# Kernel optimization log

Measured on AMD Instinct MI355X. Metric: run time of the kernel, lower is better.

## Reference

```python
import jax, jax.numpy as jnp
import numpy as np

S, H, HEADS = 2048, 1024, 16   # seq_len, hidden_size, num attention heads
E, NM, P = 256, 1024, 2048     # num entities, total mentions, num candidate pairs
PH = 1024                      # pair_hidden_size


def setup_inputs() -> dict:
    key = jax.random.key(0)
    ks = jax.random.split(key, 13)
    s = 1.0 / np.sqrt(H)
    return {
        "sequence_output": jax.random.normal(ks[0], (S, H), jnp.float32),
        "attention": jax.random.uniform(ks[1], (HEADS, S, S), jnp.float32),
        "mention_idx": jax.random.randint(ks[2], (NM,), 0, S, jnp.int32),
        "entity_ids": jnp.sort(jax.random.randint(ks[3], (NM,), 0, E, jnp.int32)),
        "pair_h": jax.random.randint(ks[4], (P,), 0, E, jnp.int32),
        "pair_t": jax.random.randint(ks[5], (P,), 0, E, jnp.int32),
        "W_head": jax.random.normal(ks[6], (H, PH), jnp.float32) * s,
        "b_head": jnp.zeros((PH,), jnp.float32),
        "W_tail": jax.random.normal(ks[7], (H, PH), jnp.float32) * s,
        "b_tail": jnp.zeros((PH,), jnp.float32),
        "W_ctx": jax.random.normal(ks[8], (H, PH), jnp.float32) * s,
        "W_bil": jax.random.normal(ks[9], (PH, PH), jnp.float32) * s,
        "b_bil": jnp.zeros((), jnp.float32),
    }


def reference(sequence_output, attention, mention_idx, entity_ids, pair_h, pair_t,
              W_head, b_head, W_tail, b_tail, W_ctx, W_bil, b_bil):
    # ---- entity aggregation: ragged segment logsumexp (embs) + segment mean (atts) ----
    vals = sequence_output[mention_idx]                               # [NM, H]
    counts = jax.ops.segment_sum(jnp.ones((NM,), vals.dtype), entity_ids, num_segments=E)
    has = counts > 0                                                  # [E]
    seg_max = jax.ops.segment_max(vals, entity_ids, num_segments=E)   # [E, H]
    seg_max = jnp.where(has[:, None], seg_max, 0.0)
    sums = jax.ops.segment_sum(jnp.exp(vals - seg_max[entity_ids]), entity_ids, num_segments=E)
    ent_emb = jnp.where(has[:, None],
                        seg_max + jnp.log(jnp.where(has[:, None], sums, 1.0)),
                        0.0)                                          # [E, H]
    m_att = jnp.transpose(attention[:, mention_idx, :], (1, 0, 2))    # [NM, HEADS, S]
    ent_att = jax.ops.segment_sum(m_att, entity_ids, num_segments=E)
    ent_att = ent_att / jnp.maximum(counts, 1.0)[:, None, None]       # [E, HEADS, S]

    # ---- pair scoring ----
    hs, ts = ent_emb[pair_h], ent_emb[pair_t]                         # [P, H]
    pair_att = (ent_att[pair_h] * ent_att[pair_t]).sum(axis=1)        # [P, S]
    pair_att = pair_att / (pair_att.sum(axis=-1, keepdims=True) + 1e-6)
    contexts = pair_att @ sequence_output                             # [P, H]
    ctx_p = contexts @ W_ctx                                          # [P, PH]
    z_s = jnp.tanh(hs @ W_head + b_head + ctx_p)
    z_o = jnp.tanh(ts @ W_tail + b_tail + ctx_p)
    logits = jnp.einsum('pi,ij,pj->p', z_s, W_bil, z_o) + b_bil       # [P]
    return logits
```

## Files before the change

kernel.cpp:

```cpp
#include <hip/hip_runtime.h>
#include <hip/hip_bf16.h>
#include <math.h>
#include <stdint.h>

#define S_LEN  2048
#define HID    1024
#define NHEADS 16
#define NE     256
#define NMEN   1024
#define NP     2048
#define PHID   1024

typedef __attribute__((ext_vector_type(8))) short bf16x8;
typedef __attribute__((ext_vector_type(4))) float f32x4;
typedef unsigned int uint;

__device__ inline void seg_bounds(const int* __restrict__ entity_ids, int e,
                                  int& start, int& end) {
    int lo = 0, hi = NMEN;
    while (lo < hi) { int mid = (lo + hi) >> 1; if (entity_ids[mid] < e) lo = mid + 1; else hi = mid; }
    start = lo;
    hi = NMEN;
    while (lo < hi) { int mid = (lo + hi) >> 1; if (entity_ids[mid] <= e) lo = mid + 1; else hi = mid; }
    end = lo;
}

__device__ __forceinline__ void load_lds16(const void* g, void* l) {
    __builtin_amdgcn_global_load_lds(
        (const __attribute__((address_space(1))) uint32_t*)g,
        (__attribute__((address_space(3))) uint32_t*)l,
        16, 0, 0);
}

__device__ __forceinline__ float bflo(uint u) { return __uint_as_float(u << 16); }
__device__ __forceinline__ float bfhi(uint u) { return __uint_as_float(u & 0xffff0000u); }
__device__ __forceinline__ uint pk2(float a, float b) {
    __hip_bfloat16 ha = __float2bfloat16(a), hb = __float2bfloat16(b);
    unsigned short ua = *(unsigned short*)&ha, ub = *(unsigned short*)&hb;
    return (uint)ua | ((uint)ub << 16);
}

__global__ void prep_ent_kernel(const float* __restrict__ seq,
                                const float* __restrict__ attention,
                                const float* __restrict__ w0, const float* __restrict__ w1,
                                const float* __restrict__ w2, const float* __restrict__ w3,
                                const int* __restrict__ mention_idx,
                                const int* __restrict__ entity_ids,
                                __hip_bfloat16* __restrict__ seqB,
                                __hip_bfloat16* __restrict__ o0, __hip_bfloat16* __restrict__ o1,
                                __hip_bfloat16* __restrict__ o2, __hip_bfloat16* __restrict__ o3,
                                uint2* __restrict__ eaB,
                                __hip_bfloat16* __restrict__ ent_emb)
{
    __shared__ float tbuf[32][33];
    __shared__ int sb[2];
    int id = blockIdx.x;
    if (id < 1024) {
        long i = (long)id * 256 + threadIdx.x;
        const float4* in4 = (const float4*)seq;
        float4 a = in4[2 * i], b = in4[2 * i + 1];
        uint4 o;
        o.x = pk2(a.x, a.y); o.y = pk2(a.z, a.w);
        o.z = pk2(b.x, b.y); o.w = pk2(b.z, b.w);
        ((uint4*)seqB)[i] = o;
        return;
    }
    if (id < 5120) {
        int t = id - 1024;
        int z = t >> 10;
        const float* in = (z == 0) ? w0 : (z == 1) ? w1 : (z == 2) ? w2 : w3;
        __hip_bfloat16* out = (z == 0) ? o0 : (z == 1) ? o1 : (z == 2) ? o2 : o3;
        int r0 = ((t >> 5) & 31) * 32, c0 = (t & 31) * 32;
        int j = threadIdx.x & 31, i0 = threadIdx.x >> 5;
        for (int i = i0; i < 32; i += 8)
            tbuf[i][j] = in[(long)(r0 + i) * 1024 + c0 + j];
        __syncthreads();
        for (int i = i0; i < 32; i += 8)
            out[(long)(c0 + i) * 1024 + r0 + j] = __float2bfloat16(tbuf[j][i]);
        return;
    }
    int t = id - 5120;
    int e = t & 255, role = t >> 8;
    if (threadIdx.x == 0) { int s, tt; seg_bounds(entity_ids, e, s, tt); sb[0] = s; sb[1] = tt; }
    __syncthreads();
    int start = sb[0], end = sb[1];

    if (role < 16) {
        const float4* att4 = (const float4*)attention;
        int h = role;
        float inv = 1.f / fmaxf((float)(end - start), 1.f);
        for (int s4 = threadIdx.x; s4 < S_LEN / 4; s4 += 256) {
            float ax = 0.f, ay = 0.f, az = 0.f, aw = 0.f;
            for (int i = start; i < end; ++i) {
                float4 v = att4[((long)h * S_LEN + mention_idx[i]) * (S_LEN / 4) + s4];
                ax += v.x; ay += v.y; az += v.z; aw += v.w;
            }
            uint2 o; o.x = pk2(ax * inv, ay * inv); o.y = pk2(az * inv, aw * inv);
            eaB[((long)e * NHEADS + h) * (S_LEN / 4) + s4] = o;
        }
    } else {
        const float4* seq4 = (const float4*)seq;
        int col4 = threadIdx.x;
        uint2 o;
        if (end <= start) {
            o.x = 0; o.y = 0;
            ((uint2*)ent_emb)[(long)e * 256 + col4] = o;
            return;
        }
        float mx = -INFINITY, my = -INFINITY, mz = -INFINITY, mw = -INFINITY;
        for (int i = start; i < end; ++i) {
            float4 v = seq4[(long)mention_idx[i] * 256 + col4];
            mx = fmaxf(mx, v.x); my = fmaxf(my, v.y); mz = fmaxf(mz, v.z); mw = fmaxf(mw, v.w);
        }
        float sx = 0.f, sy = 0.f, sz = 0.f, sw = 0.f;
        for (int i = start; i < end; ++i) {
            float4 v = seq4[(long)mention_idx[i] * 256 + col4];
            sx += expf(v.x - mx); sy += expf(v.y - my); sz += expf(v.z - mz); sw += expf(v.w - mw);
        }
        o.x = pk2(mx + logf(sx), my + logf(sy));
        o.y = pk2(mz + logf(sz), mw + logf(sw));
        ((uint2*)ent_emb)[(long)e * 256 + col4] = o;
    }
}

template <int MODE>
__device__ __forceinline__ void gemm_core(
    const __hip_bfloat16* __restrict__ A,
    const __hip_bfloat16* __restrict__ Bt,
    void* __restrict__ Cout, const float* __restrict__ zo, float* __restrict__ out,
    int M, int N, int Kstride, int kLen,
    int bx, int by, int bz,
    short (*As)[128][8], short (*Bs)[128][8])
{
    int tid = threadIdx.x;
    int lane = tid & 63, wid = tid >> 6;
    int wr = wid >> 1, wc = wid & 1;
    int bm = by * 128, bn = bx * 128;
    int kBeg = bz * kLen;

    const __hip_bfloat16* gsrc[8];
    void* ldst[8];
#pragma unroll
    for (int i = 0; i < 8; ++i) {
        int c = wid * 8 + i;
        int isA = (c < 16) ? 1 : 0;
        int cc = isA ? c : c - 16;
        int kg2 = cc >> 1, rh = cc & 1;
        gsrc[i] = (isA ? A + (long)(bm + rh * 64 + lane) * Kstride
                       : Bt + (long)(bn + rh * 64 + lane) * Kstride) + kBeg + kg2 * 8;
        ldst[i] = isA ? (void*)&As[kg2][rh * 64][0] : (void*)&Bs[kg2][rh * 64][0];
    }

    f32x4 acc[4][4] = {};
    int kg = lane >> 4, lr = lane & 15;

    for (int k0 = 0; k0 < kLen; k0 += 64) {
#pragma unroll
        for (int i = 0; i < 8; ++i)
            load_lds16(gsrc[i] + k0, ldst[i]);
        __syncthreads();
#pragma unroll
        for (int sub = 0; sub < 2; ++sub) {
            bf16x8 af[4], bfr[4];
#pragma unroll
            for (int f = 0; f < 4; ++f) {
                af[f]  = *(const bf16x8*)&As[sub * 4 + kg][wr * 64 + f * 16 + lr][0];
                bfr[f] = *(const bf16x8*)&Bs[sub * 4 + kg][wc * 64 + f * 16 + lr][0];
            }
#pragma unroll
            for (int fm = 0; fm < 4; ++fm)
#pragma unroll
                for (int fn = 0; fn < 4; ++fn)
                    acc[fm][fn] = __builtin_amdgcn_mfma_f32_16x16x32_bf16(af[fm], bfr[fn], acc[fm][fn], 0, 0, 0);
        }
        __syncthreads();
    }

    int q4 = (lane >> 4) * 4;
    if (MODE == 0) {
#pragma unroll
        for (int fm = 0; fm < 4; ++fm)
#pragma unroll
            for (int fn = 0; fn < 4; ++fn) {
                int row = bm + wr * 64 + fm * 16 + q4;
                int col = bn + wc * 64 + fn * 16 + lr;
#pragma unroll
                for (int r = 0; r < 4; ++r)
                    ((float*)Cout)[((long)bz * M + row + r) * N + col] = acc[fm][fn][r];
            }
    } else if (MODE == 1) {
#pragma unroll
        for (int fm = 0; fm < 4; ++fm)
#pragma unroll
            for (int fn = 0; fn < 4; ++fn) {
                int row = bm + wr * 64 + fm * 16 + q4;
                int col = bn + wc * 64 + fn * 16 + lr;
#pragma unroll
                for (int r = 0; r < 4; ++r)
                    ((__hip_bfloat16*)Cout)[(long)(row + r) * N + col] = __float2bfloat16(acc[fm][fn][r]);
            }
    } else {
#pragma unroll
        for (int fm = 0; fm < 4; ++fm) {
#pragma unroll
            for (int r = 0; r < 4; ++r) {
                int row = bm + wr * 64 + fm * 16 + q4 + r;
                float v = 0.f;
#pragma unroll
                for (int fn = 0; fn < 4; ++fn) {
                    int col = bn + wc * 64 + fn * 16 + lr;
                    v += acc[fm][fn][r] * zo[(long)row * N + col];
                }
                v += __shfl_xor(v, 1, 64);
                v += __shfl_xor(v, 2, 64);
                v += __shfl_xor(v, 4, 64);
                v += __shfl_xor(v, 8, 64);
                if (lr == 0) atomicAdd(out + row, v);
            }
        }
    }
}

__launch_bounds__(256)
__global__ void pair_seqw_ehet(const __hip_bfloat16* __restrict__ WctxT,
                               const __hip_bfloat16* __restrict__ seqB,
                               __hip_bfloat16* __restrict__ seqWT,
                               const __hip_bfloat16* __restrict__ embB,
                               const __hip_bfloat16* __restrict__ WhtT,
                               float* __restrict__ ehetP,
                               const uint4* __restrict__ ea,
                               const int* __restrict__ pair_h,
                               const int* __restrict__ pair_t,
                               uint4* __restrict__ patt)
{
    __shared__ short As[8][128][8];
    __shared__ short Bs[8][128][8];
    int id = blockIdx.x;
    if (id < 128) {
        gemm_core<1>(WctxT, seqB, seqWT, nullptr, nullptr,
                     PHID, S_LEN, HID, HID, id & 15, id >> 4, 0, As, Bs);
        return;
    }
    if (id < 256) {
        int u = id - 128;
        gemm_core<0>(embB, WhtT, ehetP, nullptr, nullptr,
                     NE, 2 * PHID, HID, HID / 4, u & 15, (u >> 4) & 1, u >> 5, As, Bs);
        return;
    }
    __shared__ float wsum[4];
    int p = id - 256;
    long bh = (long)pair_h[p] * NHEADS * (S_LEN / 8);
    long bt = (long)pair_t[p] * NHEADS * (S_LEN / 8);
    int s8 = threadIdx.x;
    float a0 = 0, a1 = 0, a2 = 0, a3 = 0, a4 = 0, a5 = 0, a6 = 0, a7 = 0;
#pragma unroll
    for (int h = 0; h < NHEADS; ++h) {
        uint4 xa = ea[bh + h * (S_LEN / 8) + s8];
        uint4 xb = ea[bt + h * (S_LEN / 8) + s8];
        a0 += bflo(xa.x) * bflo(xb.x); a1 += bfhi(xa.x) * bfhi(xb.x);
        a2 += bflo(xa.y) * bflo(xb.y); a3 += bfhi(xa.y) * bfhi(xb.y);
        a4 += bflo(xa.z) * bflo(xb.z); a5 += bfhi(xa.z) * bfhi(xb.z);
        a6 += bflo(xa.w) * bflo(xb.w); a7 += bfhi(xa.w) * bfhi(xb.w);
    }
    float psum = a0 + a1 + a2 + a3 + a4 + a5 + a6 + a7;
#pragma unroll
    for (int off = 32; off > 0; off >>= 1)
        psum += __shfl_down(psum, off, 64);
    int lane = threadIdx.x & 63, wid = threadIdx.x >> 6;
    if (lane == 0) wsum[wid] = psum;
    __syncthreads();
    float inv = 1.f / (wsum[0] + wsum[1] + wsum[2] + wsum[3] + 1e-6f);
    uint4 o;
    o.x = pk2(a0 * inv, a1 * inv); o.y = pk2(a2 * inv, a3 * inv);
    o.z = pk2(a4 * inv, a5 * inv); o.w = pk2(a6 * inv, a7 * inv);
    patt[(long)p * (S_LEN / 8) + s8] = o;
}

template <int MODE>
__launch_bounds__(256)
__global__ void gemm_single(const __hip_bfloat16* __restrict__ A,
                            const __hip_bfloat16* __restrict__ Bt,
                            void* __restrict__ Cout,
                            const float* __restrict__ zo,
                            float* __restrict__ out,
                            int M, int N, int Kstride, int kLen)
{
    __shared__ short As[8][128][8];
    __shared__ short Bs[8][128][8];
    gemm_core<MODE>(A, Bt, Cout, zo, out, M, N, Kstride, kLen,
                    blockIdx.x, blockIdx.y, blockIdx.z, As, Bs);
}

__global__ void zs_zo_kernel(const float* __restrict__ ctxpP,
                             const float* __restrict__ ehetP,
                             const float* __restrict__ b_head,
                             const float* __restrict__ b_tail,
                             const int* __restrict__ pair_h,
                             const int* __restrict__ pair_t,
                             __hip_bfloat16* __restrict__ zs, float* __restrict__ zo,
                             const float* __restrict__ b_bil, float* __restrict__ out)
{
    long idx = (long)blockIdx.x * 256 + threadIdx.x;
    if (idx < NP) out[idx] = b_bil[0];
    int p = (int)(idx >> 10);
    int j = (int)(idx & (PHID - 1));
    const long n = (long)NP * PHID;
    float c = ctxpP[idx] + ctxpP[n + idx] + ctxpP[2 * n + idx] + ctxpP[3 * n + idx];
    const long m = (long)NE * 2 * PHID;
    long hb = (long)pair_h[p] * 2048 + j;
    long tb = (long)pair_t[p] * 2048 + 1024 + j;
    float hs = b_head[j] + c, ts = b_tail[j] + c;
#pragma unroll
    for (int s = 0; s < 4; ++s) {
        hs += ehetP[s * m + hb];
        ts += ehetP[s * m + tb];
    }
    zs[idx] = __float2bfloat16(tanhf(hs));
    zo[idx] = tanhf(ts);
}

extern "C" void kernel_launch(void* const* d_in, const int* in_sizes, int n_in,
                              void* d_out, int out_size, void* d_ws, size_t ws_size,
                              hipStream_t stream)
{
    const float* seq        = (const float*)d_in[0];
    const float* attention  = (const float*)d_in[1];
    const int*   mention_idx= (const int*)  d_in[2];
    const int*   entity_ids = (const int*)  d_in[3];
    const int*   pair_h     = (const int*)  d_in[4];
    const int*   pair_t     = (const int*)  d_in[5];
    const float* W_head     = (const float*)d_in[6];
    const float* b_head     = (const float*)d_in[7];
    const float* W_tail     = (const float*)d_in[8];
    const float* b_tail     = (const float*)d_in[9];
    const float* W_ctx      = (const float*)d_in[10];
    const float* W_bil      = (const float*)d_in[11];
    const float* b_bil      = (const float*)d_in[12];
    float* out = (float*)d_out;

    char* w = (char*)d_ws;
    __hip_bfloat16* seqB  = (__hip_bfloat16*)(w + 0);
    __hip_bfloat16* WctxT = (__hip_bfloat16*)(w + (4l << 20));
    __hip_bfloat16* WhtT  = (__hip_bfloat16*)(w + (6l << 20));
    __hip_bfloat16* WbilT = (__hip_bfloat16*)(w + (10l << 20));
    __hip_bfloat16* embB  = (__hip_bfloat16*)(w + (12l << 20));
    __hip_bfloat16* eaB   = (__hip_bfloat16*)(w + (13l << 20));
    __hip_bfloat16* pattB = (__hip_bfloat16*)(w + (29l << 20));
    __hip_bfloat16* seqWT = (__hip_bfloat16*)(w + (37l << 20));
    __hip_bfloat16* zsB   = (__hip_bfloat16*)(w + (41l << 20));
    float* zo    = (float*)(w + (45l << 20));
    float* ctxpP = (float*)(w + (53l << 20));
    float* ehetP = (float*)(w + (85l << 20));

    prep_ent_kernel<<<9472, 256, 0, stream>>>(seq, attention, W_ctx, W_head, W_tail, W_bil,
                                              mention_idx, entity_ids,
                                              seqB, WctxT, WhtT, WhtT + (long)PHID * HID, WbilT,
                                              (uint2*)eaB, embB);

    pair_seqw_ehet<<<2304, 256, 0, stream>>>(WctxT, seqB, seqWT, embB, WhtT, ehetP,
                                             (const uint4*)eaB, pair_h, pair_t, (uint4*)pattB);

    gemm_single<0><<<dim3(8, 16, 4), 256, 0, stream>>>(pattB, seqWT, ctxpP, nullptr, nullptr,
                                                       NP, PHID, S_LEN, S_LEN / 4);

    zs_zo_kernel<<<8192, 256, 0, stream>>>(ctxpP, ehetP, b_head, b_tail, pair_h, pair_t,
                                           zsB, zo, b_bil, out);

    gemm_single<2><<<dim3(8, 16, 2), 256, 0, stream>>>(zsB, WbilT, nullptr, zo, out,
                                                       NP, PHID, HID, HID / 2);
}
```

Measured before the change: 145.8 us.

## Shrink intermediates to bf16, fold ehet split-K reduce into ctxp GEMM launch

The split-K partial outputs of the context GEMM are now stored as bf16 instead of fp32. The four ehet partials are pre-reduced by extra blocks in the same launch as that GEMM, and the blocks are remapped in a swizzled order. zs_zo is vectorised to four elements per thread and writes zo in bf16. W_bil is no longer transposed; the bilinear GEMM instead uses zo as the A operand and untransposed W_bil, with zs as the epilogue vector. The aim is to cut HBM traffic and the transpose work, at the cost of extra bf16 rounding on the partial sums and on zo.

```diff
diff --git a/kernel.cpp b/kernel.cpp
--- a/kernel.cpp
+++ b/kernel.cpp
@@ -43,12 +43,12 @@
 __global__ void prep_ent_kernel(const float* __restrict__ seq,
                                 const float* __restrict__ attention,
                                 const float* __restrict__ w0, const float* __restrict__ w1,
-                                const float* __restrict__ w2, const float* __restrict__ w3,
+                                const float* __restrict__ w2, const float* __restrict__ wbil,
                                 const int* __restrict__ mention_idx,
                                 const int* __restrict__ entity_ids,
                                 __hip_bfloat16* __restrict__ seqB,
                                 __hip_bfloat16* __restrict__ o0, __hip_bfloat16* __restrict__ o1,
-                                __hip_bfloat16* __restrict__ o2, __hip_bfloat16* __restrict__ o3,
+                                __hip_bfloat16* __restrict__ o2, __hip_bfloat16* __restrict__ obil,
                                 uint2* __restrict__ eaB,
                                 __hip_bfloat16* __restrict__ ent_emb)
 {
@@ -65,11 +65,11 @@
         ((uint4*)seqB)[i] = o;
         return;
     }
-    if (id < 5120) {
+    if (id < 4096) {
         int t = id - 1024;
         int z = t >> 10;
-        const float* in = (z == 0) ? w0 : (z == 1) ? w1 : (z == 2) ? w2 : w3;
-        __hip_bfloat16* out = (z == 0) ? o0 : (z == 1) ? o1 : (z == 2) ? o2 : o3;
+        const float* in = (z == 0) ? w0 : (z == 1) ? w1 : w2;
+        __hip_bfloat16* out = (z == 0) ? o0 : (z == 1) ? o1 : o2;
         int r0 = ((t >> 5) & 31) * 32, c0 = (t & 31) * 32;
         int j = threadIdx.x & 31, i0 = threadIdx.x >> 5;
         for (int i = i0; i < 32; i += 8)
@@ -79,7 +79,17 @@
             out[(long)(c0 + i) * 1024 + r0 + j] = __float2bfloat16(tbuf[j][i]);
         return;
     }
-    int t = id - 5120;
+    if (id < 4608) {
+        long i = (long)(id - 4096) * 256 + threadIdx.x;
+        const float4* in4 = (const float4*)wbil;
+        float4 a = in4[2 * i], b = in4[2 * i + 1];
+        uint4 o;
+        o.x = pk2(a.x, a.y); o.y = pk2(a.z, a.w);
+        o.z = pk2(b.x, b.y); o.w = pk2(b.z, b.w);
+        ((uint4*)obil)[i] = o;
+        return;
+    }
+    int t = id - 4608;
     int e = t & 255, role = t >> 8;
     if (threadIdx.x == 0) { int s, tt; seg_bounds(entity_ids, e, s, tt); sb[0] = s; sb[1] = tt; }
     __syncthreads();
@@ -127,7 +137,7 @@
 __device__ __forceinline__ void gemm_core(
     const __hip_bfloat16* __restrict__ A,
     const __hip_bfloat16* __restrict__ Bt,
-    void* __restrict__ Cout, const float* __restrict__ zo, float* __restrict__ out,
+    void* __restrict__ Cout, const __hip_bfloat16* __restrict__ zvec, float* __restrict__ out,
     int M, int N, int Kstride, int kLen,
     int bx, int by, int bz,
     short (*As)[128][8], short (*Bs)[128][8])
@@ -199,6 +209,17 @@
                 for (int r = 0; r < 4; ++r)
                     ((__hip_bfloat16*)Cout)[(long)(row + r) * N + col] = __float2bfloat16(acc[fm][fn][r]);
             }
+    } else if (MODE == 3) {
+#pragma unroll
+        for (int fm = 0; fm < 4; ++fm)
+#pragma unroll
+            for (int fn = 0; fn < 4; ++fn) {
+                int row = bm + wr * 64 + fm * 16 + q4;
+                int col = bn + wc * 64 + fn * 16 + lr;
+#pragma unroll
+                for (int r = 0; r < 4; ++r)
+                    ((__hip_bfloat16*)Cout)[((long)bz * M + row + r) * N + col] = __float2bfloat16(acc[fm][fn][r]);
+            }
     } else {
 #pragma unroll
         for (int fm = 0; fm < 4; ++fm) {
@@ -209,7 +230,7 @@
 #pragma unroll
                 for (int fn = 0; fn < 4; ++fn) {
                     int col = bn + wc * 64 + fn * 16 + lr;
-                    v += acc[fm][fn][r] * zo[(long)row * N + col];
+                    v += acc[fm][fn][r] * __bfloat162float(zvec[(long)row * N + col]);
                 }
                 v += __shfl_xor(v, 1, 64);
                 v += __shfl_xor(v, 2, 64);
@@ -276,47 +297,90 @@
     patt[(long)p * (S_LEN / 8) + s8] = o;
 }
 
+__launch_bounds__(256)
+__global__ void gemm_ctxp_reduce(const __hip_bfloat16* __restrict__ pattB,
+                                 const __hip_bfloat16* __restrict__ seqWT,
+                                 __hip_bfloat16* __restrict__ ctxpB,
+                                 const float* __restrict__ ehetP,
+                                 float* __restrict__ ehet)
+{
+    __shared__ short As[8][128][8];
+    __shared__ short Bs[8][128][8];
+    int id = blockIdx.x;
+    if (id < 512) {
+        int f = (id & 7) * 64 + (id >> 3);
+        int bx = f >> 6, inner = f & 63;
+        int by = inner & 15, bz = inner >> 4;
+        gemm_core<3>(pattB, seqWT, ctxpB, nullptr, nullptr,
+                     NP, PHID, S_LEN, S_LEN / 4, bx, by, bz, As, Bs);
+        return;
+    }
+    long i = (long)(id - 512) * 2048 + (long)threadIdx.x * 8;
+    const long n = (long)NE * 2 * PHID;
+    float4 s0 = make_float4(0.f, 0.f, 0.f, 0.f), s1 = s0;
+#pragma unroll
+    for (int s = 0; s < 4; ++s) {
+        float4 a = *(const float4*)&ehetP[s * n + i];
+        float4 b = *(const float4*)&ehetP[s * n + i + 4];
+        s0.x += a.x; s0.y += a.y; s0.z += a.z; s0.w += a.w;
+        s1.x += b.x; s1.y += b.y; s1.z += b.z; s1.w += b.w;
+    }
+    *(float4*)&ehet[i] = s0;
+    *(float4*)&ehet[i + 4] = s1;
+}
+
+__global__ void zs_zo_kernel(const __hip_bfloat16* __restrict__ ctxpB,
+                             const float* __restrict__ ehet,
+                             const float* __restrict__ b_head,
+                             const float* __restrict__ b_tail,
+                             const int* __restrict__ pair_h,
+                             const int* __restrict__ pair_t,
+                             __hip_bfloat16* __restrict__ zs,
+                             __hip_bfloat16* __restrict__ zo,
+                             const float* __restrict__ b_bil, float* __restrict__ out)
+{
+    long base = ((long)blockIdx.x * 256 + threadIdx.x) * 4;
+    if (base < NP) {
+        float bb = b_bil[0];
+#pragma unroll
+        for (int i = 0; i < 4; ++i) out[base + i] = bb;
+    }
+    int p = (int)(base >> 10);
+    int j = (int)(base & (PHID - 1));
+    const long n = (long)NP * PHID;
+    float c0 = 0.f, c1 = 0.f, c2 = 0.f, c3 = 0.f;
+#pragma unroll
+    for (int s = 0; s < 4; ++s) {
+        uint2 u = *(const uint2*)&ctxpB[s * n + base];
+        c0 += bflo(u.x); c1 += bfhi(u.x); c2 += bflo(u.y); c3 += bfhi(u.y);
+    }
+    float4 eh = *(const float4*)&ehet[(long)pair_h[p] * 2048 + j];
+    float4 et = *(const float4*)&ehet[(long)pair_t[p] * 2048 + 1024 + j];
+    float4 bh = *(const float4*)&b_head[j];
+    float4 bt = *(const float4*)&b_tail[j];
+    float h0 = tanhf(eh.x + bh.x + c0), h1 = tanhf(eh.y + bh.y + c1);
+    float h2 = tanhf(eh.z + bh.z + c2), h3 = tanhf(eh.w + bh.w + c3);
+    float t0 = tanhf(et.x + bt.x + c0), t1 = tanhf(et.y + bt.y + c1);
+    float t2 = tanhf(et.z + bt.z + c2), t3 = tanhf(et.w + bt.w + c3);
+    uint2 ozs; ozs.x = pk2(h0, h1); ozs.y = pk2(h2, h3);
+    uint2 ozo; ozo.x = pk2(t0, t1); ozo.y = pk2(t2, t3);
+    *(uint2*)&zs[base] = ozs;
+    *(uint2*)&zo[base] = ozo;
+}
+
 template <int MODE>
 __launch_bounds__(256)
 __global__ void gemm_single(const __hip_bfloat16* __restrict__ A,
                             const __hip_bfloat16* __restrict__ Bt,
                             void* __restrict__ Cout,
-                            const float* __restrict__ zo,
+                            const __hip_bfloat16* __restrict__ zvec,
                             float* __restrict__ out,
                             int M, int N, int Kstride, int kLen)
 {
     __shared__ short As[8][128][8];
     __shared__ short Bs[8][128][8];
-    gemm_core<MODE>(A, Bt, Cout, zo, out, M, N, Kstride, kLen,
+    gemm_core<MODE>(A, Bt, Cout, zvec, out, M, N, Kstride, kLen,
                     blockIdx.x, blockIdx.y, blockIdx.z, As, Bs);
-}
-
-__global__ void zs_zo_kernel(const float* __restrict__ ctxpP,
-                             const float* __restrict__ ehetP,
-                             const float* __restrict__ b_head,
-                             const float* __restrict__ b_tail,
-                             const int* __restrict__ pair_h,
-                             const int* __restrict__ pair_t,
-                             __hip_bfloat16* __restrict__ zs, float* __restrict__ zo,
-                             const float* __restrict__ b_bil, float* __restrict__ out)
-{
-    long idx = (long)blockIdx.x * 256 + threadIdx.x;
-    if (idx < NP) out[idx] = b_bil[0];
-    int p = (int)(idx >> 10);
-    int j = (int)(idx & (PHID - 1));
-    const long n = (long)NP * PHID;
-    float c = ctxpP[idx] + ctxpP[n + idx] + ctxpP[2 * n + idx] + ctxpP[3 * n + idx];
-    const long m = (long)NE * 2 * PHID;
-    long hb = (long)pair_h[p] * 2048 + j;
-    long tb = (long)pair_t[p] * 2048 + 1024 + j;
-    float hs = b_head[j] + c, ts = b_tail[j] + c;
-#pragma unroll
-    for (int s = 0; s < 4; ++s) {
-        hs += ehetP[s * m + hb];
-        ts += ehetP[s * m + tb];
-    }
-    zs[idx] = __float2bfloat16(tanhf(hs));
-    zo[idx] = tanhf(ts);
 }
 
 extern "C" void kernel_launch(void* const* d_in, const int* in_sizes, int n_in,
@@ -342,30 +406,30 @@
     __hip_bfloat16* seqB  = (__hip_bfloat16*)(w + 0);
     __hip_bfloat16* WctxT = (__hip_bfloat16*)(w + (4l << 20));
     __hip_bfloat16* WhtT  = (__hip_bfloat16*)(w + (6l << 20));
-    __hip_bfloat16* WbilT = (__hip_bfloat16*)(w + (10l << 20));
+    __hip_bfloat16* WbilB = (__hip_bfloat16*)(w + (10l << 20));
     __hip_bfloat16* embB  = (__hip_bfloat16*)(w + (12l << 20));
     __hip_bfloat16* eaB   = (__hip_bfloat16*)(w + (13l << 20));
     __hip_bfloat16* pattB = (__hip_bfloat16*)(w + (29l << 20));
     __hip_bfloat16* seqWT = (__hip_bfloat16*)(w + (37l << 20));
     __hip_bfloat16* zsB   = (__hip_bfloat16*)(w + (41l << 20));
-    float* zo    = (float*)(w + (45l << 20));
-    float* ctxpP = (float*)(w + (53l << 20));
-    float* ehetP = (float*)(w + (85l << 20));
-
-    prep_ent_kernel<<<9472, 256, 0, stream>>>(seq, attention, W_ctx, W_head, W_tail, W_bil,
+    __hip_bfloat16* zoB   = (__hip_bfloat16*)(w + (45l << 20));
+    __hip_bfloat16* ctxpB = (__hip_bfloat16*)(w + (49l << 20));
+    float* ehetP = (float*)(w + (65l << 20));
+    float* ehet  = (float*)(w + (73l << 20));
+
+    prep_ent_kernel<<<8960, 256, 0, stream>>>(seq, attention, W_ctx, W_head, W_tail, W_bil,
                                               mention_idx, entity_ids,
-                                              seqB, WctxT, WhtT, WhtT + (long)PHID * HID, WbilT,
+                                              seqB, WctxT, WhtT, WhtT + (long)PHID * HID, WbilB,
                                               (uint2*)eaB, embB);
 
     pair_seqw_ehet<<<2304, 256, 0, stream>>>(WctxT, seqB, seqWT, embB, WhtT, ehetP,
                                              (const uint4*)eaB, pair_h, pair_t, (uint4*)pattB);
 
-    gemm_single<0><<<dim3(8, 16, 4), 256, 0, stream>>>(pattB, seqWT, ctxpP, nullptr, nullptr,
-                                                       NP, PHID, S_LEN, S_LEN / 4);
-
-    zs_zo_kernel<<<8192, 256, 0, stream>>>(ctxpP, ehetP, b_head, b_tail, pair_h, pair_t,
-                                           zsB, zo, b_bil, out);
-
-    gemm_single<2><<<dim3(8, 16, 2), 256, 0, stream>>>(zsB, WbilT, nullptr, zo, out,
+    gemm_ctxp_reduce<<<768, 256, 0, stream>>>(pattB, seqWT, ctxpB, ehetP, ehet);
+
+    zs_zo_kernel<<<2048, 256, 0, stream>>>(ctxpB, ehet, b_head, b_tail, pair_h, pair_t,
+                                           zsB, zoB, b_bil, out);
+
+    gemm_single<2><<<dim3(8, 16, 2), 256, 0, stream>>>(zoB, WbilB, nullptr, zsB, out,
                                                        NP, PHID, HID, HID / 2);
 }
```

New measurement: 139.8 us. 4.1% less time.
